# Kernel optimization log

Measured on AMD Instinct MI355X. Metric: run time of the kernel, lower is better.

Reference implementation:

```python
import jax, jax.numpy as jnp
import numpy as np

V, D, T_MAX, H, L = 32000, 1024, 1024, 16, 8
HD = D // H
DFF = 4 * D
EPS = 1e-5


def _pos_encoding(T, d_model, dtype=jnp.float32):
    pos = jnp.arange(T, dtype=jnp.float32)[:, None]                      # [T,1]
    div = jnp.exp(jnp.arange(0, d_model, 2, dtype=jnp.float32) * (-jnp.log(10000.0) / d_model))
    pe = jnp.zeros((T, d_model), dtype=jnp.float32)
    pe = pe.at[:, 0::2].set(jnp.sin(pos * div))
    pe = pe.at[:, 1::2].set(jnp.cos(pos * div))
    return pe.astype(dtype)


def _layernorm(x, g, b):
    mu = jnp.mean(x, axis=-1, keepdims=True)
    var = jnp.mean(jnp.square(x - mu), axis=-1, keepdims=True)
    return (x - mu) * jax.lax.rsqrt(var + EPS) * g + b


def setup_inputs() -> dict:
    key = jax.random.key(0)
    ks = jax.random.split(key, 9)
    s = 0.02
    return {
        "idx": jax.random.randint(ks[0], (2, 1024), 0, V),
        "embed": jax.random.normal(ks[1], (V, D), jnp.float32) * s,
        "Wqkv": jax.random.normal(ks[2], (L, D, 3 * D), jnp.float32) * s,
        "Wproj": jax.random.normal(ks[3], (L, D, D), jnp.float32) * s,
        "bproj": jnp.zeros((L, D), jnp.float32),
        "ln1_g": jnp.ones((L, D), jnp.float32),
        "ln1_b": jnp.zeros((L, D), jnp.float32),
        "ln2_g": jnp.ones((L, D), jnp.float32),
        "ln2_b": jnp.zeros((L, D), jnp.float32),
        "W1": jax.random.normal(ks[4], (L, D, DFF), jnp.float32) * s,
        "b1": jnp.zeros((L, DFF), jnp.float32),
        "W2": jax.random.normal(ks[5], (L, DFF, D), jnp.float32) * s,
        "b2": jnp.zeros((L, D), jnp.float32),
        "lnf_g": jnp.ones((D,), jnp.float32),
        "lnf_b": jnp.zeros((D,), jnp.float32),
        "Whead": jax.random.normal(ks[6], (D, V), jnp.float32) * s,
    }


def _attn(x, Wqkv, Wproj, bproj):
    B, T, C = x.shape
    qkv = (x @ Wqkv).reshape(B, T, 3, H, HD)
    q, k, v = [jnp.transpose(qkv[:, :, i], (0, 2, 1, 3)) for i in range(3)]  # [B,H,T,HD]
    scores = jnp.einsum('bhqd,bhkd->bhqk', q, k) * (HD ** -0.5)
    mask = jnp.tril(jnp.ones((T, T), dtype=bool))
    scores = jnp.where(mask, scores, -jnp.inf)
    w = jax.nn.softmax(scores, axis=-1)
    out = jnp.einsum('bhqk,bhkd->bhqd', w, v)
    out = jnp.transpose(out, (0, 2, 1, 3)).reshape(B, T, C)
    return out @ Wproj + bproj


def reference(idx, embed, Wqkv, Wproj, bproj, ln1_g, ln1_b, ln2_g, ln2_b,
              W1, b1, W2, b2, lnf_g, lnf_b, Whead):
    idx = idx[:, :T_MAX]
    T = idx.shape[1]
    x = embed[idx] + _pos_encoding(T, D)[None]          # [B,T,D]
    for l in range(L):
        x = x + _attn(_layernorm(x, ln1_g[l], ln1_b[l]), Wqkv[l], Wproj[l], bproj[l])
        h = _layernorm(x, ln2_g[l], ln2_b[l])
        x = x + jax.nn.relu(h @ W1[l] + b1[l]) @ W2[l] + b2[l]
    x = _layernorm(x, lnf_g, lnf_b)
    return x @ Whead                                     # [B,T,V]
```

## Files before the change

kernel.cpp:

```cpp
#include <hip/hip_runtime.h>
#include <cstddef>

#define DM    1024
#define TSEQ  1024
#define NB    2
#define NHEAD 16
#define HDIM  64
#define NLAYER 8
#define DFFN  4096
#define NVOC  32000
#define NROWS (NB*TSEQ)

typedef __attribute__((ext_vector_type(8))) short short8;
typedef __attribute__((ext_vector_type(4))) float f32x4;

static __device__ __forceinline__ unsigned short f2bf(float f) {
    union { float f; unsigned int u; } v; v.f = f;
    unsigned int r = v.u + 0x7FFF + ((v.u >> 16) & 1);
    return (unsigned short)(r >> 16);
}

static __device__ __forceinline__ void gload_lds16(const void* g, void* l) {
    __builtin_amdgcn_global_load_lds(
        (const __attribute__((address_space(1))) unsigned int*)g,
        (__attribute__((address_space(3))) unsigned int*)l, 16, 0, 0);
}

__global__ __launch_bounds__(256)
void embed_pos_k(const int* __restrict__ idx, const float* __restrict__ embed,
                 float* __restrict__ x)
{
    int row = blockIdx.x;
    int t   = row & (TSEQ - 1);
    int tid = threadIdx.x;
    int token = idx[row];
    const float* er = embed + (size_t)token * DM;
    float* xr = x + (size_t)row * DM;
    const float neg_ln1e4_over_d = -9.210340371976184f / (float)DM;
    for (int i = tid; i < DM; i += 256) {
        int half = i >> 1;
        float div = expf((float)(2 * half) * neg_ln1e4_over_d);
        float ang = (float)t * div;
        float pe = (i & 1) ? cosf(ang) : sinf(ang);
        xr[i] = er[i] + pe;
    }
}

__global__ __launch_bounds__(256)
void layernorm_k(const float* __restrict__ x, const float* __restrict__ g,
                 const float* __restrict__ b, unsigned short* __restrict__ y)
{
    int row = blockIdx.x;
    int tid = threadIdx.x;
    const float* xr = x + (size_t)row * DM;
    unsigned short* yr = y + (size_t)row * DM;
    float vals[4];
    float s = 0.f;
    #pragma unroll
    for (int i = 0; i < 4; ++i) { vals[i] = xr[tid + 256 * i]; s += vals[i]; }
    __shared__ float red[256];
    red[tid] = s; __syncthreads();
    for (int st = 128; st > 0; st >>= 1) {
        if (tid < st) red[tid] += red[tid + st];
        __syncthreads();
    }
    float mu = red[0] * (1.f / DM);
    __syncthreads();
    float v = 0.f;
    #pragma unroll
    for (int i = 0; i < 4; ++i) { float d = vals[i] - mu; v += d * d; }
    red[tid] = v; __syncthreads();
    for (int st = 128; st > 0; st >>= 1) {
        if (tid < st) red[tid] += red[tid + st];
        __syncthreads();
    }
    float rstd = rsqrtf(red[0] * (1.f / DM) + 1e-5f);
    #pragma unroll
    for (int i = 0; i < 4; ++i) {
        int c = tid + 256 * i;
        yr[c] = f2bf((vals[i] - mu) * rstd * g[c] + b[c]);
    }
}

__global__ __launch_bounds__(256)
void reduce_ln_k(const float* __restrict__ P, int nsplit, const float* __restrict__ bias,
                 float* __restrict__ X, const float* __restrict__ g,
                 const float* __restrict__ b, unsigned short* __restrict__ XN)
{
    const int row = blockIdx.x;
    const int tid = threadIdx.x;
    const size_t off4 = (size_t)row * 256 + tid;
    const size_t tot4 = (size_t)NROWS * 256;

    float4 v = *((const float4*)X + off4);
    float4 bb = *((const float4*)bias + tid);
    v.x += bb.x; v.y += bb.y; v.z += bb.z; v.w += bb.w;
    for (int s = 0; s < nsplit; ++s) {
        float4 p = *((const float4*)P + s * tot4 + off4);
        v.x += p.x; v.y += p.y; v.z += p.z; v.w += p.w;
    }
    *((float4*)X + off4) = v;

    __shared__ float red[256];
    red[tid] = v.x + v.y + v.z + v.w;
    __syncthreads();
    for (int st = 128; st > 0; st >>= 1) {
        if (tid < st) red[tid] += red[tid + st];
        __syncthreads();
    }
    float mu = red[0] * (1.f / DM);
    __syncthreads();
    float4 d = make_float4(v.x - mu, v.y - mu, v.z - mu, v.w - mu);
    red[tid] = d.x * d.x + d.y * d.y + d.z * d.z + d.w * d.w;
    __syncthreads();
    for (int st = 128; st > 0; st >>= 1) {
        if (tid < st) red[tid] += red[tid + st];
        __syncthreads();
    }
    float rstd = rsqrtf(red[0] * (1.f / DM) + 1e-5f);
    float4 gg = *((const float4*)g + tid);
    float4 bbn = *((const float4*)b + tid);
    unsigned short o[4];
    o[0] = f2bf(d.x * rstd * gg.x + bbn.x);
    o[1] = f2bf(d.y * rstd * gg.y + bbn.y);
    o[2] = f2bf(d.z * rstd * gg.z + bbn.z);
    o[3] = f2bf(d.w * rstd * gg.w + bbn.w);
    *(ushort4*)(XN + (size_t)row * DM + tid * 4) = *(ushort4*)o;
}

__global__ __launch_bounds__(256)
void convt_k(const float* __restrict__ src, unsigned short* __restrict__ dst,
             int K, int N)
{
    __shared__ __align__(16) unsigned short T[64][72];
    const int tid = threadIdx.x;
    const int n0 = blockIdx.x * 64, k0 = blockIdx.y * 64;
    const float* s = src + (size_t)blockIdx.z * K * N;
    unsigned short* d = dst + (size_t)blockIdx.z * K * N;
    #pragma unroll
    for (int q = 0; q < 4; ++q) {
        int f4 = tid + q * 256;
        int kk = f4 >> 4, nn = (f4 & 15) * 4;
        float4 v = *(const float4*)(s + (size_t)(k0 + kk) * N + n0 + nn);
        int swz = ((nn >> 2) & 7) << 3;
        T[nn + 0][kk ^ swz] = f2bf(v.x);
        T[nn + 1][kk ^ swz] = f2bf(v.y);
        T[nn + 2][kk ^ swz] = f2bf(v.z);
        T[nn + 3][kk ^ swz] = f2bf(v.w);
    }
    __syncthreads();
    #pragma unroll
    for (int q = 0; q < 2; ++q) {
        int s8 = tid + q * 256;
        int nn = s8 >> 3, kc = (s8 & 7) * 8;
        int swz = ((nn >> 2) & 7) << 3;
        *(short8*)(d + (size_t)(n0 + nn) * K + k0 + kc) =
            *(const short8*)&T[nn][kc ^ swz];
    }
}

template<int BM, bool OUT_BF16>
__global__ __launch_bounds__(256)
void gemm_tn(const unsigned short* __restrict__ A, const unsigned short* __restrict__ BT,
             const float* __restrict__ bias, const float* __restrict__ residual,
             void* __restrict__ Cout, int M, int N, int K, int KS, int relu)
{
    constexpr int FR = BM / 32;
    constexpr int RPW = BM / 4;
    constexpr int NI = BM / 64;
    __shared__ __align__(16) unsigned short As[2][BM][32];
    __shared__ __align__(16) unsigned short Bs[2][BM][32];

    const int tid = threadIdx.x;
    const int lane = tid & 63;
    const int w = tid >> 6;
    const int wr = w >> 1, wc = w & 1;
    const int l16 = lane & 15, g = lane >> 4;

    const int nby = M / BM;
    const int nwg = (N / BM) * nby;
    const int cpx = nwg >> 3;
    const int bid = blockIdx.x;
    const int sbid = (bid & 7) * cpx + (bid >> 3);
    const int row0 = (sbid % nby) * BM;
    const int col0 = (sbid / nby) * BM;

    const int srow = w * RPW + (lane >> 2);
    const int scol = (((lane & 3) ^ ((lane >> 3) & 3)) << 3);
    const int rslot = ((g ^ ((l16 >> 1) & 3)) << 3);

    const unsigned short* ga = A  + (size_t)(row0 + srow) * KS + (size_t)blockIdx.y * K + scol;
    const unsigned short* gb = BT + (size_t)(col0 + srow) * KS + (size_t)blockIdx.y * K + scol;

    f32x4 acc[FR][FR] = {};

    #pragma unroll
    for (int i = 0; i < NI; ++i) {
        gload_lds16(ga + (size_t)(i * 16) * KS, &As[0][srow + i * 16][(lane & 3) << 3]);
        gload_lds16(gb + (size_t)(i * 16) * KS, &Bs[0][srow + i * 16][(lane & 3) << 3]);
    }
    __syncthreads();

    int cur = 0;
    for (int k0 = 0; k0 < K; k0 += 32) {
        if (k0 + 32 < K) {
            #pragma unroll
            for (int i = 0; i < NI; ++i) {
                gload_lds16(ga + k0 + 32 + (size_t)(i * 16) * KS, &As[cur ^ 1][srow + i * 16][(lane & 3) << 3]);
                gload_lds16(gb + k0 + 32 + (size_t)(i * 16) * KS, &Bs[cur ^ 1][srow + i * 16][(lane & 3) << 3]);
            }
        }
        short8 af[FR], bf[FR];
        #pragma unroll
        for (int i = 0; i < FR; ++i)
            af[i] = *(const short8*)&As[cur][wr * (BM / 2) + i * 16 + l16][rslot];
        #pragma unroll
        for (int j = 0; j < FR; ++j)
            bf[j] = *(const short8*)&Bs[cur][wc * (BM / 2) + j * 16 + l16][rslot];
        #pragma unroll
        for (int i = 0; i < FR; ++i)
            #pragma unroll
            for (int j = 0; j < FR; ++j)
                acc[i][j] = __builtin_amdgcn_mfma_f32_16x16x32_bf16(af[i], bf[j], acc[i][j], 0, 0, 0);
        __syncthreads();
        cur ^= 1;
    }

    float* Cf = (float*)Cout + (size_t)blockIdx.y * M * N;
    #pragma unroll
    for (int i = 0; i < FR; ++i) {
        #pragma unroll
        for (int j = 0; j < FR; ++j) {
            #pragma unroll
            for (int r = 0; r < 4; ++r) {
                int row = row0 + wr * (BM / 2) + i * 16 + g * 4 + r;
                int col = col0 + wc * (BM / 2) + j * 16 + l16;
                float v = acc[i][j][r];
                if (bias)     v += bias[col];
                if (residual) v += residual[(size_t)row * N + col];
                if (relu)     v = fmaxf(v, 0.f);
                if (OUT_BF16) ((unsigned short*)Cout)[(size_t)row * N + col] = f2bf(v);
                else          Cf[(size_t)row * N + col] = v;
            }
        }
    }
}

__global__ __launch_bounds__(256)
void attn_flash_k(const unsigned short* __restrict__ qkv, unsigned short* __restrict__ out)
{
    __shared__ unsigned short Ks[64][72];
    __shared__ unsigned short Vt[64][72];
    __shared__ unsigned short Ps[4][16][72];

    const int tid = threadIdx.x;
    const int lane = tid & 63;
    const int w = tid >> 6;
    const int l16 = lane & 15, g = lane >> 4;
    const int h = blockIdx.y;
    const int b = blockIdx.z;

    const size_t rstr = 3 * DM;
    const unsigned short* base = qkv + (size_t)b * TSEQ * rstr + h * HDIM;

    const int krow0 = tid >> 3, kcol = (tid & 7) * 8;
    const int vkv = tid & 63, vdg = tid >> 6;

    short8 kreg0, kreg1, vreg0, vreg1;

    #pragma unroll
    for (int pass = 0; pass < 2; ++pass) {
        const int qb = pass ? (15 - (int)blockIdx.x) : (int)blockIdx.x;
        const int q0 = qb * 64;
        const int nt = qb + 1;

        const int qrow_w = q0 + w * 16 + l16;
        short8 aq0 = *(const short8*)(base + (size_t)qrow_w * rstr + g * 8);
        short8 aq1 = *(const short8*)(base + (size_t)qrow_w * rstr + 32 + g * 8);

        f32x4 acc_o[4] = {};
        float m_r[4] = {-INFINITY, -INFINITY, -INFINITY, -INFINITY};
        float l_r[4] = {};

        {
            const unsigned short* kb = base + DM;
            kreg0 = *(const short8*)(kb + (size_t)krow0 * rstr + kcol);
            kreg1 = *(const short8*)(kb + (size_t)(32 + krow0) * rstr + kcol);
            const unsigned short* vsrc = base + (size_t)vkv * rstr + 2 * DM + vdg * 16;
            vreg0 = *(const short8*)vsrc;
            vreg1 = *(const short8*)(vsrc + 8);
        }

        for (int t = 0; t < nt; ++t) {
            *(short8*)&Ks[krow0][kcol] = kreg0;
            *(short8*)&Ks[32 + krow0][kcol] = kreg1;
            #pragma unroll
            for (int j = 0; j < 8; ++j) Vt[vdg * 16 + j][vkv] = (unsigned short)vreg0[j];
            #pragma unroll
            for (int j = 0; j < 8; ++j) Vt[vdg * 16 + 8 + j][vkv] = (unsigned short)vreg1[j];
            __syncthreads();

            if (t + 1 < nt) {
                const int kv0n = (t + 1) * 64;
                const unsigned short* kb = base + (size_t)kv0n * rstr + DM;
                kreg0 = *(const short8*)(kb + (size_t)krow0 * rstr + kcol);
                kreg1 = *(const short8*)(kb + (size_t)(32 + krow0) * rstr + kcol);
                const unsigned short* vsrc = base + (size_t)(kv0n + vkv) * rstr + 2 * DM + vdg * 16;
                vreg0 = *(const short8*)vsrc;
                vreg1 = *(const short8*)(vsrc + 8);
            }

            const int kv0 = t * 64;
            f32x4 acc_s[4] = {};
            #pragma unroll
            for (int ks = 0; ks < 4; ++ks) {
                short8 bk0 = *(const short8*)&Ks[ks * 16 + l16][g * 8];
                short8 bk1 = *(const short8*)&Ks[ks * 16 + l16][32 + g * 8];
                acc_s[ks] = __builtin_amdgcn_mfma_f32_16x16x32_bf16(aq0, bk0, acc_s[ks], 0, 0, 0);
                acc_s[ks] = __builtin_amdgcn_mfma_f32_16x16x32_bf16(aq1, bk1, acc_s[ks], 0, 0, 0);
            }
            const bool need_mask = (kv0 + 63 > q0 + w * 16);
            float alpha[4];
            #pragma unroll
            for (int r = 0; r < 4; ++r) {
                const int q_abs = q0 + w * 16 + g * 4 + r;
                float s[4];
                #pragma unroll
                for (int ks = 0; ks < 4; ++ks) {
                    s[ks] = acc_s[ks][r] * 0.125f;
                    if (need_mask && (kv0 + ks * 16 + l16 > q_abs)) s[ks] = -INFINITY;
                }
                float pm = fmaxf(fmaxf(s[0], s[1]), fmaxf(s[2], s[3]));
                #pragma unroll
                for (int msk = 1; msk <= 8; msk <<= 1)
                    pm = fmaxf(pm, __shfl_xor(pm, msk));
                float mnew = fmaxf(m_r[r], pm);
                alpha[r] = __expf(m_r[r] - mnew);
                m_r[r] = mnew;
                float p[4], psum = 0.f;
                #pragma unroll
                for (int ks = 0; ks < 4; ++ks) {
                    p[ks] = (s[ks] == -INFINITY) ? 0.f : __expf(s[ks] - mnew);
                    psum += p[ks];
                }
                #pragma unroll
                for (int msk = 1; msk <= 8; msk <<= 1)
                    psum += __shfl_xor(psum, msk);
                l_r[r] = l_r[r] * alpha[r] + psum;
                #pragma unroll
                for (int ks = 0; ks < 4; ++ks)
                    Ps[w][g * 4 + r][ks * 16 + l16] = f2bf(p[ks]);
            }
            #pragma unroll
            for (int ds = 0; ds < 4; ++ds)
                #pragma unroll
                for (int r = 0; r < 4; ++r)
                    acc_o[ds][r] *= alpha[r];
            short8 ap0 = *(const short8*)&Ps[w][l16][g * 8];
            short8 ap1 = *(const short8*)&Ps[w][l16][32 + g * 8];
            #pragma unroll
            for (int ds = 0; ds < 4; ++ds) {
                short8 bv0 = *(const short8*)&Vt[ds * 16 + l16][g * 8];
                short8 bv1 = *(const short8*)&Vt[ds * 16 + l16][32 + g * 8];
                acc_o[ds] = __builtin_amdgcn_mfma_f32_16x16x32_bf16(ap0, bv0, acc_o[ds], 0, 0, 0);
                acc_o[ds] = __builtin_amdgcn_mfma_f32_16x16x32_bf16(ap1, bv1, acc_o[ds], 0, 0, 0);
            }
            __syncthreads();
        }

        #pragma unroll
        for (int ds = 0; ds < 4; ++ds)
            #pragma unroll
            for (int r = 0; r < 4; ++r) {
                int row = q0 + w * 16 + g * 4 + r;
                out[((size_t)b * TSEQ + row) * DM + h * HDIM + ds * 16 + l16] =
                    f2bf(acc_o[ds][r] * (1.f / l_r[r]));
            }
    }
}

extern "C" void kernel_launch(void* const* d_in, const int* in_sizes, int n_in,
                              void* d_out, int out_size, void* d_ws, size_t ws_size,
                              hipStream_t stream)
{
    const int*   idx    = (const int*)  d_in[0];
    const float* embed  = (const float*)d_in[1];
    const float* Wqkv   = (const float*)d_in[2];
    const float* Wproj  = (const float*)d_in[3];
    const float* bproj  = (const float*)d_in[4];
    const float* ln1_g  = (const float*)d_in[5];
    const float* ln1_b  = (const float*)d_in[6];
    const float* ln2_g  = (const float*)d_in[7];
    const float* ln2_b  = (const float*)d_in[8];
    const float* W1     = (const float*)d_in[9];
    const float* b1     = (const float*)d_in[10];
    const float* W2     = (const float*)d_in[11];
    const float* b2     = (const float*)d_in[12];
    const float* lnf_g  = (const float*)d_in[13];
    const float* lnf_b  = (const float*)d_in[14];
    const float* Whead  = (const float*)d_in[15];
    float* out = (float*)d_out;

    float* X = (float*)d_ws;
    float* PK = X + (size_t)NROWS * DM;
    unsigned short* u = (unsigned short*)(PK + (size_t)4 * NROWS * DM);
    unsigned short* XN     = u;  u += (size_t)NROWS * DM;
    unsigned short* QKVb   = u;  u += (size_t)NROWS * 3 * DM;
    unsigned short* ATT    = u;  u += (size_t)NROWS * DM;
    unsigned short* FFH    = u;  u += (size_t)NROWS * DFFN;
    unsigned short* WqkvT  = u;  u += (size_t)NLAYER * 3 * DM * DM;
    unsigned short* WprojT = u;  u += (size_t)NLAYER * DM * DM;
    unsigned short* W1T    = u;  u += (size_t)NLAYER * DFFN * DM;
    unsigned short* W2T    = u;  u += (size_t)NLAYER * DM * DFFN;
    unsigned short* WheadT = u;  u += (size_t)NVOC * DM;

    convt_k<<<dim3(3 * DM / 64, DM / 64, NLAYER), 256, 0, stream>>>(Wqkv,  WqkvT,  DM,   3 * DM);
    convt_k<<<dim3(DM / 64,     DM / 64, NLAYER), 256, 0, stream>>>(Wproj, WprojT, DM,   DM);
    convt_k<<<dim3(DFFN / 64,   DM / 64, NLAYER), 256, 0, stream>>>(W1,    W1T,    DM,   DFFN);
    convt_k<<<dim3(DM / 64,   DFFN / 64, NLAYER), 256, 0, stream>>>(W2,    W2T,    DFFN, DM);
    convt_k<<<dim3(NVOC / 64,   DM / 64, 1),      256, 0, stream>>>(Whead, WheadT, DM,   NVOC);

    embed_pos_k<<<NROWS, 256, 0, stream>>>(idx, embed, X);
    layernorm_k<<<NROWS, 256, 0, stream>>>(X, ln1_g, ln1_b, XN);

    for (int l = 0; l < NLAYER; ++l) {
        const unsigned short* wqkvT_l  = WqkvT  + (size_t)l * 3 * DM * DM;
        const unsigned short* wprojT_l = WprojT + (size_t)l * DM * DM;
        const unsigned short* w1T_l    = W1T    + (size_t)l * DFFN * DM;
        const unsigned short* w2T_l    = W2T    + (size_t)l * DM * DFFN;
        const float* bproj_l = bproj + (size_t)l * DM;
        const float* b1_l = b1 + (size_t)l * DFFN;
        const float* b2_l = b2 + (size_t)l * DM;

        {
            int nwg = (NROWS / 128) * (3 * DM / 128);
            gemm_tn<128, true><<<nwg, 256, 0, stream>>>(XN, wqkvT_l, nullptr, nullptr,
                                                        QKVb, NROWS, 3 * DM, DM, DM, 0);
        }
        {
            dim3 grid(TSEQ / 128, NHEAD, NB);
            attn_flash_k<<<grid, 256, 0, stream>>>(QKVb, ATT);
        }
        {
            dim3 grid((NROWS / 128) * (DM / 128), 2);
            gemm_tn<128, false><<<grid, 256, 0, stream>>>(ATT, wprojT_l, nullptr, nullptr,
                                                          PK, NROWS, DM, 512, DM, 0);
            reduce_ln_k<<<NROWS, 256, 0, stream>>>(PK, 2, bproj_l, X,
                                                   ln2_g + (size_t)l * DM,
                                                   ln2_b + (size_t)l * DM, XN);
        }
        {
            int nwg = (NROWS / 128) * (DFFN / 128);
            gemm_tn<128, true><<<nwg, 256, 0, stream>>>(XN, w1T_l, b1_l, nullptr,
                                                        FFH, NROWS, DFFN, DM, DM, 1);
        }
        {
            dim3 grid((NROWS / 128) * (DM / 128), 4);
            gemm_tn<128, false><<<grid, 256, 0, stream>>>(FFH, w2T_l, nullptr, nullptr,
                                                          PK, NROWS, DM, 1024, DFFN, 0);
            const float* ng = (l + 1 < NLAYER) ? ln1_g + (size_t)(l + 1) * DM : lnf_g;
            const float* nb = (l + 1 < NLAYER) ? ln1_b + (size_t)(l + 1) * DM : lnf_b;
            reduce_ln_k<<<NROWS, 256, 0, stream>>>(PK, 4, b2_l, X, ng, nb, XN);
        }
    }

    {
        int nwg = (NROWS / 128) * (NVOC / 128);
        gemm_tn<128, false><<<nwg, 256, 0, stream>>>(XN, WheadT, nullptr, nullptr,
                                                     out, NROWS, NVOC, DM, DM, 0);
    }
}
```

Measured before the change: 1.846 ms.

## Add 256x128 triple-buffered bf16 GEMM for QKV, FFN1 and head

Introduces a new 512-thread GEMM kernel with 256x128 output tiles, a 64-wide K step, and a three-stage LDS ring filled by direct global-to-LDS loads with XOR swizzling. It also remaps workgroup IDs for locality. It replaces the 128x128 kernel for the QKV projection, the first FFN matmul and the vocabulary head. The aim is more data reuse per tile and deeper latency hiding. The cost is higher LDS use (about 144KB) and register pressure, which lowers occupancy and may reduce wave counts for the smaller GEMMs.

```diff
diff --git a/kernel.cpp b/kernel.cpp
--- a/kernel.cpp
+++ b/kernel.cpp
@@ -156,6 +156,108 @@
         int swz = ((nn >> 2) & 7) << 3;
         *(short8*)(d + (size_t)(n0 + nn) * K + k0 + kc) =
             *(const short8*)&T[nn][kc ^ swz];
+    }
+}
+
+template<bool OUT_BF16>
+__global__ __launch_bounds__(512)
+void gemm256(const unsigned short* __restrict__ A, const unsigned short* __restrict__ BT,
+             const float* __restrict__ bias, void* __restrict__ Cout,
+             int M, int N, int K, int relu)
+{
+    __shared__ __align__(16) unsigned short AS[3][256][64];
+    __shared__ __align__(16) unsigned short BS[3][128][64];
+
+    const int tid  = threadIdx.x;
+    const int lane = tid & 63;
+    const int w    = tid >> 6;
+    const int wm = w >> 1, wn = w & 1;
+    const int l16 = lane & 15, g = lane >> 4;
+
+    const int nby = M / 256;
+    const int nwg = nby * (N / 128);
+    const int cpx = nwg >> 3;
+    const int bid = (int)blockIdx.x;
+    const int sbid = (bid & 7) * cpx + (bid >> 3);
+    const int row0 = (sbid % nby) * 256;
+    const int col0 = (sbid / nby) * 128;
+
+    const int srow = tid >> 3;
+    const int schunk = ((tid & 7) ^ (srow & 7)) << 3;
+    const unsigned short* ga = A  + (size_t)(row0 + srow) * K + schunk;
+    const unsigned short* gb = BT + (size_t)(col0 + srow) * K + schunk;
+    const int NT = K >> 6;
+
+    f32x4 acc[4][4] = {};
+
+    #pragma unroll
+    for (int t = 0; t < 2; ++t) {
+        #pragma unroll
+        for (int i = 0; i < 4; ++i)
+            gload_lds16(ga + t * 64 + (size_t)(i * 64) * K,
+                        (unsigned short*)AS[t] + i * 4096 + tid * 8);
+        #pragma unroll
+        for (int i = 0; i < 2; ++i)
+            gload_lds16(gb + t * 64 + (size_t)(i * 64) * K,
+                        (unsigned short*)BS[t] + i * 4096 + tid * 8);
+    }
+    asm volatile("s_waitcnt vmcnt(6)" ::: "memory");
+    __builtin_amdgcn_s_barrier();
+
+    for (int t = 0; t < NT; ++t) {
+        const int rs = t % 3;
+        if (t + 2 < NT) {
+            const int ss = (t + 2) % 3;
+            #pragma unroll
+            for (int i = 0; i < 4; ++i)
+                gload_lds16(ga + (t + 2) * 64 + (size_t)(i * 64) * K,
+                            (unsigned short*)AS[ss] + i * 4096 + tid * 8);
+            #pragma unroll
+            for (int i = 0; i < 2; ++i)
+                gload_lds16(gb + (t + 2) * 64 + (size_t)(i * 64) * K,
+                            (unsigned short*)BS[ss] + i * 4096 + tid * 8);
+        }
+        #pragma unroll
+        for (int s = 0; s < 2; ++s) {
+            short8 af[4], bf[4];
+            #pragma unroll
+            for (int i = 0; i < 4; ++i) {
+                const int ar = wm * 64 + i * 16 + l16;
+                af[i] = *(const short8*)&AS[rs][ar][((((s << 2) | g) ^ (l16 & 7)) << 3)];
+            }
+            #pragma unroll
+            for (int j = 0; j < 4; ++j) {
+                const int br = wn * 64 + j * 16 + l16;
+                bf[j] = *(const short8*)&BS[rs][br][((((s << 2) | g) ^ (l16 & 7)) << 3)];
+            }
+            __builtin_amdgcn_s_setprio(1);
+            #pragma unroll
+            for (int i = 0; i < 4; ++i)
+                #pragma unroll
+                for (int j = 0; j < 4; ++j)
+                    acc[i][j] = __builtin_amdgcn_mfma_f32_16x16x32_bf16(af[i], bf[j], acc[i][j], 0, 0, 0);
+            __builtin_amdgcn_s_setprio(0);
+        }
+        if (t + 2 < NT) { asm volatile("s_waitcnt vmcnt(6)" ::: "memory"); }
+        else            { asm volatile("s_waitcnt vmcnt(0)" ::: "memory"); }
+        __builtin_amdgcn_s_barrier();
+    }
+
+    #pragma unroll
+    for (int i = 0; i < 4; ++i) {
+        #pragma unroll
+        for (int j = 0; j < 4; ++j) {
+            #pragma unroll
+            for (int r = 0; r < 4; ++r) {
+                int row = row0 + wm * 64 + i * 16 + g * 4 + r;
+                int col = col0 + wn * 64 + j * 16 + l16;
+                float v = acc[i][j][r];
+                if (bias) v += bias[col];
+                if (relu) v = fmaxf(v, 0.f);
+                if (OUT_BF16) ((unsigned short*)Cout)[(size_t)row * N + col] = f2bf(v);
+                else          ((float*)Cout)[(size_t)row * N + col] = v;
+            }
+        }
     }
 }
 
@@ -433,9 +535,9 @@
         const float* b2_l = b2 + (size_t)l * DM;
 
         {
-            int nwg = (NROWS / 128) * (3 * DM / 128);
-            gemm_tn<128, true><<<nwg, 256, 0, stream>>>(XN, wqkvT_l, nullptr, nullptr,
-                                                        QKVb, NROWS, 3 * DM, DM, DM, 0);
+            int nwg = (NROWS / 256) * (3 * DM / 128);
+            gemm256<true><<<nwg, 512, 0, stream>>>(XN, wqkvT_l, nullptr,
+                                                   QKVb, NROWS, 3 * DM, DM, 0);
         }
         {
             dim3 grid(TSEQ / 128, NHEAD, NB);
@@ -450,9 +552,9 @@
                                                    ln2_b + (size_t)l * DM, XN);
         }
         {
-            int nwg = (NROWS / 128) * (DFFN / 128);
-            gemm_tn<128, true><<<nwg, 256, 0, stream>>>(XN, w1T_l, b1_l, nullptr,
-                                                        FFH, NROWS, DFFN, DM, DM, 1);
+            int nwg = (NROWS / 256) * (DFFN / 128);
+            gemm256<true><<<nwg, 512, 0, stream>>>(XN, w1T_l, b1_l,
+                                                   FFH, NROWS, DFFN, DM, 1);
         }
         {
             dim3 grid((NROWS / 128) * (DM / 128), 4);
@@ -465,8 +567,8 @@
     }
 
     {
-        int nwg = (NROWS / 128) * (NVOC / 128);
-        gemm_tn<128, false><<<nwg, 256, 0, stream>>>(XN, WheadT, nullptr, nullptr,
-                                                     out, NROWS, NVOC, DM, DM, 0);
-    }
-}
+        int nwg = (NROWS / 256) * (NVOC / 128);
+        gemm256<false><<<nwg, 512, 0, stream>>>(XN, WheadT, nullptr,
+                                                out, NROWS, NVOC, DM, 0);
+    }
+}
```

Result: no change. 1.819 ms (-1.5%).

## Triple-buffer GEMM LDS tiles with vmcnt waits and a single barrier

Applied to the files above, without the earlier changes.

Replaces the GEMM's double-buffered LDS K-loop with a three-stage ring that prefetches two tiles ahead. Each iteration waits with an explicit s_waitcnt vmcnt and a raw s_barrier instead of a trailing __syncthreads, so global-to-LDS loads overlap more MFMA work. It also raises wave priority around the MFMA block with s_setprio. The cost is 1.5x the LDS per block, which may reduce occupancy. The hardcoded vmcnt(4) assumes four loads per stage, which is only correct when BM=128 (NI=2); smaller tiles could race.

```diff
diff --git a/kernel.cpp b/kernel.cpp
--- a/kernel.cpp
+++ b/kernel.cpp
@@ -168,8 +168,8 @@
     constexpr int FR = BM / 32;
     constexpr int RPW = BM / 4;
     constexpr int NI = BM / 64;
-    __shared__ __align__(16) unsigned short As[2][BM][32];
-    __shared__ __align__(16) unsigned short Bs[2][BM][32];
+    __shared__ __align__(16) unsigned short As[3][BM][32];
+    __shared__ __align__(16) unsigned short Bs[3][BM][32];
 
     const int tid = threadIdx.x;
     const int lane = tid & 63;
@@ -188,42 +188,53 @@
     const int srow = w * RPW + (lane >> 2);
     const int scol = (((lane & 3) ^ ((lane >> 3) & 3)) << 3);
     const int rslot = ((g ^ ((l16 >> 1) & 3)) << 3);
+    const int ldst = (lane & 3) << 3;
 
     const unsigned short* ga = A  + (size_t)(row0 + srow) * KS + (size_t)blockIdx.y * K + scol;
     const unsigned short* gb = BT + (size_t)(col0 + srow) * KS + (size_t)blockIdx.y * K + scol;
 
     f32x4 acc[FR][FR] = {};
-
-    #pragma unroll
-    for (int i = 0; i < NI; ++i) {
-        gload_lds16(ga + (size_t)(i * 16) * KS, &As[0][srow + i * 16][(lane & 3) << 3]);
-        gload_lds16(gb + (size_t)(i * 16) * KS, &Bs[0][srow + i * 16][(lane & 3) << 3]);
-    }
-    __syncthreads();
-
-    int cur = 0;
-    for (int k0 = 0; k0 < K; k0 += 32) {
-        if (k0 + 32 < K) {
+    const int NT = K >> 5;
+
+    #pragma unroll
+    for (int tt = 0; tt < 2; ++tt) {
+        #pragma unroll
+        for (int i = 0; i < NI; ++i) {
+            gload_lds16(ga + tt * 32 + (size_t)(i * 16) * KS, &As[tt][srow + i * 16][ldst]);
+            gload_lds16(gb + tt * 32 + (size_t)(i * 16) * KS, &Bs[tt][srow + i * 16][ldst]);
+        }
+    }
+
+    for (int t = 0; t < NT; ++t) {
+        const int rb = t % 3;
+        if (t + 1 < NT) { asm volatile("s_waitcnt vmcnt(4)" ::: "memory"); }
+        else            { asm volatile("s_waitcnt vmcnt(0)" ::: "memory"); }
+        __builtin_amdgcn_s_barrier();
+
+        if (t + 2 < NT) {
+            const int wb = (t + 2) % 3;
+            const int ko = (t + 2) * 32;
             #pragma unroll
             for (int i = 0; i < NI; ++i) {
-                gload_lds16(ga + k0 + 32 + (size_t)(i * 16) * KS, &As[cur ^ 1][srow + i * 16][(lane & 3) << 3]);
-                gload_lds16(gb + k0 + 32 + (size_t)(i * 16) * KS, &Bs[cur ^ 1][srow + i * 16][(lane & 3) << 3]);
-            }
-        }
+                gload_lds16(ga + ko + (size_t)(i * 16) * KS, &As[wb][srow + i * 16][ldst]);
+                gload_lds16(gb + ko + (size_t)(i * 16) * KS, &Bs[wb][srow + i * 16][ldst]);
+            }
+        }
+
         short8 af[FR], bf[FR];
         #pragma unroll
         for (int i = 0; i < FR; ++i)
-            af[i] = *(const short8*)&As[cur][wr * (BM / 2) + i * 16 + l16][rslot];
+            af[i] = *(const short8*)&As[rb][wr * (BM / 2) + i * 16 + l16][rslot];
         #pragma unroll
         for (int j = 0; j < FR; ++j)
-            bf[j] = *(const short8*)&Bs[cur][wc * (BM / 2) + j * 16 + l16][rslot];
+            bf[j] = *(const short8*)&Bs[rb][wc * (BM / 2) + j * 16 + l16][rslot];
+        __builtin_amdgcn_s_setprio(1);
         #pragma unroll
         for (int i = 0; i < FR; ++i)
             #pragma unroll
             for (int j = 0; j < FR; ++j)
                 acc[i][j] = __builtin_amdgcn_mfma_f32_16x16x32_bf16(af[i], bf[j], acc[i][j], 0, 0, 0);
-        __syncthreads();
-        cur ^= 1;
+        __builtin_amdgcn_s_setprio(0);
     }
 
     float* Cf = (float*)Cout + (size_t)blockIdx.y * M * N;
```

Result: no change. 1.877 ms (+1.6%).
